# Optimization experiments

Measured on AMD Instinct MI355X. Metric: run time of the kernel, lower is better.

The kernel has to match this reference:

```python
import jax, jax.numpy as jnp
import numpy as np

B, C, Q, T, D = 16, 6, 256, 256, 256
NUM_IDS = 300
IMG_H = IMG_W = 512


def setup_inputs() -> dict:
    key = jax.random.key(0)
    ks = jax.random.split(key, 8)
    det_tokens = jax.random.normal(ks[0], (B, C, Q, D), jnp.float32)
    det_scores = jax.random.uniform(ks[1], (B, C, Q), jnp.float32)
    det_boxes = jax.random.uniform(ks[2], (B, C, Q, 4), jnp.float32)
    assoc = jax.nn.softmax(jax.random.normal(ks[3], (B, C, Q, T), jnp.float32), axis=-1)
    cam_mask = jax.random.uniform(ks[4], (B, C)) < 0.9
    target_mask = jax.random.uniform(ks[5], (B, C, Q)) < 0.5
    ids = jax.random.randint(ks[6], (B, C, Q), 0, NUM_IDS)
    boxes = jax.random.uniform(ks[7], (B, C, Q, 4), jnp.float32) * IMG_W
    return {"det_tokens": det_tokens, "det_scores": det_scores, "det_boxes": det_boxes,
            "assoc": assoc, "boxes": boxes, "cam_mask": cam_mask,
            "target_mask": target_mask, "ids": ids, "img_h": IMG_H, "img_w": IMG_W}


def _masked_mean(x, m):
    w = m.astype(x.dtype)
    return (x * w).sum() / jnp.maximum(w.sum(), 1.0)


def _pack(ids, target_mask, cam_mask, q_count):
    # Vectorized version of _query_ids_from_targets: stable-compact valid targets
    # to the front of the query axis (preserves original order, as boolean indexing does).
    order = jnp.argsort(jnp.where(target_mask, 0, 1), axis=-1, stable=True)  # valid first
    sids = jnp.take_along_axis(ids, order, axis=-1)[..., :q_count]
    count = target_mask.sum(axis=-1)  # [B,C]
    qvalid = (jnp.arange(q_count)[None, None, :] < count[..., None]) & cam_mask[..., None]
    qids = jnp.where(qvalid, sids, -1)
    return qids, qvalid, order


def reference(det_tokens, det_scores, det_boxes, assoc, boxes, cam_mask, target_mask, ids, img_h, img_w):
    Bq, Cc, Qn, Tn = assoc.shape
    qids, qvalid, order = _pack(ids, target_mask, cam_mask, Qn)

    # det_norm
    det_norm = jnp.mean(det_tokens ** 2)

    # detector supervision (masked BCE on scores + masked L1 on boxes)
    norm = jnp.array([img_w, img_h, img_w, img_h], det_boxes.dtype)
    box_gt = boxes / norm  # [B,C,maxT,4]
    sboxes = jnp.take_along_axis(box_gt, order[..., None], axis=2)[:, :, :Qn]
    obj_target = qvalid.astype(det_scores.dtype)
    box_target = jnp.where(qvalid[..., None], jnp.clip(sboxes, 0.0, 1.0), 0.0)
    p = jnp.clip(det_scores, 1e-6, 1.0 - 1e-6)
    bce = -(obj_target * jnp.log(p) + (1.0 - obj_target) * jnp.log1p(-p))
    cam3 = jnp.broadcast_to(cam_mask[:, :, None], bce.shape)
    score_loss = _masked_mean(bce, cam3)
    box_loss = _masked_mean(jnp.abs(det_boxes - box_target),
                            jnp.broadcast_to(qvalid[..., None], det_boxes.shape))
    det_supervision = score_loss + box_loss

    # assoc entropy (masked by camera validity)
    logp_full = jnp.log(jnp.maximum(assoc, 1e-8))
    entropy = -(logp_full * assoc).sum(-1)  # [B,C,Q]
    assoc_entropy_loss = _masked_mean(entropy, jnp.broadcast_to(cam_mask[:, :, None], entropy.shape))

    # assoc supervised NLL over track slots
    slots = jnp.remainder(jnp.maximum(qids, 0), Tn)  # [B,C,Q]
    nll = -jnp.take_along_axis(logp_full, slots[..., None], axis=-1)[..., 0]
    assoc_pair_loss = _masked_mean(nll, qvalid)

    # cross-view consistency: broadcasted id-equality replaces quadruple python loop
    eq = qids[:, :, None, :, None] == qids[:, None, :, None, :]       # [B,c1,c2,q1,q2]
    pv = qvalid[:, :, None, :, None] & qvalid[:, None, :, None, :]
    tri = jnp.triu(jnp.ones((Cc, Cc), bool), 1)[None, :, :, None, None]  # c1 < c2
    M = (eq & pv & tri).astype(assoc.dtype)
    cnt = M.sum(-1)  # [B,c1,c2,q1]
    peer = jnp.einsum('bcdqp,bdpt->bcdqt', M, assoc) / jnp.maximum(cnt, 1.0)[..., None]
    ref = assoc[:, :, None, :, :]
    term = jnp.mean((ref - peer) ** 2, axis=-1)  # per-pair MSE over track slots
    assoc_consistency = _masked_mean(term, cnt > 0)

    total = det_norm + det_supervision + assoc_entropy_loss + assoc_pair_loss + assoc_consistency
    return total, det_norm, det_supervision, assoc_entropy_loss, assoc_pair_loss, assoc_consistency
```

## Files before the change

### kernel.cpp

```cpp
#include <hip/hip_runtime.h>
#include <math.h>

#define BB 16
#define CC 6
#define QQ 256
#define TT 256
#define DD 256
#define NPAIR 15
#define NBC (BB * CC)
#define BIG_BLOCKS (NBC * 16)
#define CONS_BLOCKS (BB * NPAIR * 4)


__device__ __forceinline__ float block_sum256(float v, float* s_red) {
    #pragma unroll
    for (int off = 32; off > 0; off >>= 1) v += __shfl_xor(v, off, 64);
    __syncthreads();
    if ((threadIdx.x & 63) == 0) s_red[threadIdx.x >> 6] = v;
    __syncthreads();
    return s_red[0] + s_red[1] + s_red[2] + s_red[3];
}

__device__ __forceinline__ int read_bool(const void* p, int idx, int fmt) {
    if (fmt == 2) return ((const float*)p)[idx] != 0.0f;
    if (fmt == 1) return ((const unsigned char*)p)[idx] != 0;
    return ((const int*)p)[idx] != 0;
}

__global__ __launch_bounds__(256)
void k_pack(const float* __restrict__ det_scores,
            const float* __restrict__ det_boxes,
            const float* __restrict__ assoc,
            const float* __restrict__ boxes,
            const void* __restrict__ cam_raw,
            const void* __restrict__ tm_raw,
            const int* __restrict__ ids,
            const int* __restrict__ img_h_p,
            const int* __restrict__ img_w_p,
            unsigned char* __restrict__ cam_c,
            int* __restrict__ qids,
            float* __restrict__ packPart) {
    const int bc = blockIdx.x;
    const int t = threadIdx.x;
    const int lane = t & 63, wv = t >> 6;
    __shared__ int s_cf, s_cm, s_wsum[4];
    __shared__ int s_sids[QQ];
    __shared__ float s_red[4];

    if (t == 0) { s_cf = 0; s_cm = 0; }
    __syncthreads();
    {
        uint4 w = ((const uint4*)tm_raw)[t];
        unsigned int u4[4] = {w.x, w.y, w.z, w.w};
        int cf = 0, cm = 0;
        #pragma unroll
        for (int k = 0; k < 4; k++) {
            cf += ((u4[k] >> 24) == 0x3Fu);
            cm += ((u4[k] & 0xFFFFFF00u) != 0u);
        }
        if (cf) atomicAdd(&s_cf, cf);
        if (cm) atomicAdd(&s_cm, cm);
    }
    __syncthreads();
    const int fmt = (s_cf > 16) ? 2 : ((s_cm > 0) ? 1 : 0);

    const int cam = read_bool(cam_raw, bc, fmt);
    const int tm  = read_bool(tm_raw, bc * QQ + t, fmt);
    if (t == 0) cam_c[bc] = (unsigned char)cam;

    int v = tm;
    #pragma unroll
    for (int off = 1; off < 64; off <<= 1) {
        int u = __shfl_up(v, off, 64);
        if (lane >= off) v += u;
    }
    if (lane == 63) s_wsum[wv] = v;
    __syncthreads();
    const int count = s_wsum[0] + s_wsum[1] + s_wsum[2] + s_wsum[3];
    int woff = 0;
    #pragma unroll
    for (int k = 0; k < 3; k++) woff += (k < wv) ? s_wsum[k] : 0;
    const int excl = woff + v - tm;
    const int rank = tm ? excl : (count + (t - excl));

    s_sids[rank] = ids[bc * QQ + t];
    __syncthreads();

    const int j = t;
    const int qv = (j < count) && cam;
    const int qid = qv ? s_sids[j] : -1;
    qids[bc * QQ + j] = qid;

    float score_sum = 0.0f, box_sum = 0.0f, pair_sum = 0.0f;

    if (cam) {
        float p = det_scores[(size_t)bc * QQ + j];
        p = fminf(fmaxf(p, 1e-6f), 1.0f - 1e-6f);
        score_sum = (j < count) ? -__logf(p) : -__logf(1.0f - p);
    }
    if (qv) {
        int slot = qid & (TT - 1);
        float a = assoc[((size_t)bc * QQ + j) * TT + slot];
        pair_sum = -__logf(fmaxf(a, 1e-8f));
    }
    if (tm && cam) {
        const int jj = rank;
        const float iw = (float)img_w_p[0], ih = (float)img_h_p[0];
        const float* bx = boxes + ((size_t)bc * QQ + t) * 4;
        const float* db = det_boxes + ((size_t)bc * QQ + jj) * 4;
        float b0 = fminf(fmaxf(bx[0] / iw, 0.0f), 1.0f);
        float b1 = fminf(fmaxf(bx[1] / ih, 0.0f), 1.0f);
        float b2 = fminf(fmaxf(bx[2] / iw, 0.0f), 1.0f);
        float b3 = fminf(fmaxf(bx[3] / ih, 0.0f), 1.0f);
        box_sum = fabsf(db[0] - b0) + fabsf(db[1] - b1) +
                  fabsf(db[2] - b2) + fabsf(db[3] - b3);
    }

    float vs = block_sum256(score_sum, s_red);
    float vb = block_sum256(box_sum, s_red);
    float vp = block_sum256(pair_sum, s_red);
    if (t == 0) {
        float* row = packPart + bc * 8;
        row[0] = vs; row[1] = vb; row[2] = vp;
        row[3] = cam ? (float)count : 0.0f;
        row[4] = (float)cam;
    }
}

__global__ __launch_bounds__(256)
void k_big(const float4* __restrict__ tok, const float4* __restrict__ asc,
           const unsigned char* __restrict__ cam_c, float* __restrict__ bigPart) {
    const int blk = blockIdx.x;
    const int bc = blk >> 4;
    const int t = threadIdx.x;
    const long base = (long)bc * 16384 + (long)(blk & 15) * 1024 + t;

    float4 t0 = tok[base], t1 = tok[base + 256],
           t2 = tok[base + 512], t3 = tok[base + 768];
    float ss = t0.x * t0.x + t0.y * t0.y + t0.z * t0.z + t0.w * t0.w
             + t1.x * t1.x + t1.y * t1.y + t1.z * t1.z + t1.w * t1.w
             + t2.x * t2.x + t2.y * t2.y + t2.z * t2.z + t2.w * t2.w
             + t3.x * t3.x + t3.y * t3.y + t3.z * t3.z + t3.w * t3.w;

    float ent = 0.0f;
    if (cam_c[bc]) {
        float4 a0 = asc[base], a1 = asc[base + 256],
               a2 = asc[base + 512], a3 = asc[base + 768];
        ent -= a0.x * __logf(fmaxf(a0.x, 1e-8f)) + a0.y * __logf(fmaxf(a0.y, 1e-8f))
             + a0.z * __logf(fmaxf(a0.z, 1e-8f)) + a0.w * __logf(fmaxf(a0.w, 1e-8f));
        ent -= a1.x * __logf(fmaxf(a1.x, 1e-8f)) + a1.y * __logf(fmaxf(a1.y, 1e-8f))
             + a1.z * __logf(fmaxf(a1.z, 1e-8f)) + a1.w * __logf(fmaxf(a1.w, 1e-8f));
        ent -= a2.x * __logf(fmaxf(a2.x, 1e-8f)) + a2.y * __logf(fmaxf(a2.y, 1e-8f))
             + a2.z * __logf(fmaxf(a2.z, 1e-8f)) + a2.w * __logf(fmaxf(a2.w, 1e-8f));
        ent -= a3.x * __logf(fmaxf(a3.x, 1e-8f)) + a3.y * __logf(fmaxf(a3.y, 1e-8f))
             + a3.z * __logf(fmaxf(a3.z, 1e-8f)) + a3.w * __logf(fmaxf(a3.w, 1e-8f));
    }

    __shared__ float s_red[4];
    float vss = block_sum256(ss, s_red);
    float vent = block_sum256(ent, s_red);
    if (t == 0) { bigPart[blk * 2] = vss; bigPart[blk * 2 + 1] = vent; }
}

__global__ __launch_bounds__(256)
void k_cons(const float* __restrict__ assoc, const int* __restrict__ qids,
            float* __restrict__ consPart) {
    const int blk = blockIdx.x;
    const int qg = blk & 3;
    const int bp = blk >> 2;
    const int b = bp / NPAIR;
    int pi = bp % NPAIR;
    int c = 0, d = 1;
    {
        int k = pi;
        for (c = 0; c < CC - 1; c++) {
            int span = CC - 1 - c;
            if (k < span) { d = c + 1 + k; break; }
            k -= span;
        }
    }
    const int t = threadIdx.x, lane = t & 63, wv = t >> 6;
    __shared__ int s_qc[64];
    __shared__ int s_qd[QQ];
    __shared__ float s_wred[4];
    __shared__ int s_wnval[4];
    if (t < 64) s_qc[t] = qids[(b * CC + c) * QQ + qg * 64 + t];
    s_qd[t] = qids[(b * CC + d) * QQ + t];
    __syncthreads();

    const int qd0 = s_qd[lane];
    const int qd1 = s_qd[64 + lane];
    const int qd2 = s_qd[128 + lane];
    const int qd3 = s_qd[192 + lane];
    const float4* assoc_c = (const float4*)(assoc + (size_t)(b * CC + c) * QQ * TT);
    const float4* assoc_d = (const float4*)(assoc + (size_t)(b * CC + d) * QQ * TT);

    float tot = 0.0f;
    int nval = 0;
    for (int qi = 0; qi < 16; qi++) {
        const int qloc = wv * 16 + qi;
        const int id = s_qc[qloc];
        if (id < 0) continue;
        unsigned long long m0 = __ballot(qd0 == id);
        unsigned long long m1 = __ballot(qd1 == id);
        unsigned long long m2 = __ballot(qd2 == id);
        unsigned long long m3 = __ballot(qd3 == id);
        int cnt = __popcll(m0) + __popcll(m1) + __popcll(m2) + __popcll(m3);
        if (cnt == 0) continue;
        const int q = qg * 64 + qloc;
        float4 r = assoc_c[(size_t)q * (TT / 4) + lane];
        float ax = 0.0f, ay = 0.0f, az = 0.0f, aw = 0.0f;
        unsigned long long mm[4] = {m0, m1, m2, m3};
        #pragma unroll
        for (int kk = 0; kk < 4; kk++) {
            unsigned long long m = mm[kk];
            while (m) {
                int p = kk * 64 + __builtin_ctzll(m);
                m &= m - 1;
                float4 vv = assoc_d[(size_t)p * (TT / 4) + lane];
                ax += vv.x; ay += vv.y; az += vv.z; aw += vv.w;
            }
        }
        float inv = 1.0f / (float)cnt;
        float dx = r.x - ax * inv, dy = r.y - ay * inv;
        float dz = r.z - az * inv, dw = r.w - aw * inv;
        tot += dx * dx + dy * dy + dz * dz + dw * dw;
        nval++;
    }
    #pragma unroll
    for (int off = 32; off > 0; off >>= 1) tot += __shfl_xor(tot, off, 64);
    if (lane == 0) { s_wred[wv] = tot; s_wnval[wv] = nval; }
    __syncthreads();
    if (t == 0) {
        float csum = s_wred[0] + s_wred[1] + s_wred[2] + s_wred[3];
        int n4 = s_wnval[0] + s_wnval[1] + s_wnval[2] + s_wnval[3];
        consPart[blk * 2] = csum * (1.0f / TT);
        consPart[blk * 2 + 1] = (float)n4;
    }
}

__global__ __launch_bounds__(256)
void k_fin(const float* __restrict__ packPart, const float* __restrict__ bigPart,
           const float* __restrict__ consPart, float* __restrict__ out) {
    const int t = threadIdx.x;
    __shared__ float s_red[4];
    float sc = 0, bx = 0, pr = 0, qv = 0, cm = 0;
    if (t < NBC) {
        const float* row = packPart + t * 8;
        sc = row[0]; bx = row[1]; pr = row[2]; qv = row[3]; cm = row[4];
    }
    float ss = 0, ent = 0;
    for (int i = t; i < BIG_BLOCKS; i += 256) {
        ss += bigPart[2 * i]; ent += bigPart[2 * i + 1];
    }
    float cons = 0, nval = 0;
    for (int i = t; i < CONS_BLOCKS; i += 256) {
        cons += consPart[2 * i]; nval += consPart[2 * i + 1];
    }
    sc = block_sum256(sc, s_red);
    bx = block_sum256(bx, s_red);
    pr = block_sum256(pr, s_red);
    qv = block_sum256(qv, s_red);
    cm = block_sum256(cm, s_red);
    ss = block_sum256(ss, s_red);
    ent = block_sum256(ent, s_red);
    cons = block_sum256(cons, s_red);
    nval = block_sum256(nval, s_red);
    if (t == 0) {
        float det_norm = ss / (float)((long)BB * CC * QQ * DD);
        float denom_cam = fmaxf(cm * (float)QQ, 1.0f);
        float score_loss = sc / denom_cam;
        float box_loss = bx / fmaxf(4.0f * qv, 1.0f);
        float det_sup = score_loss + box_loss;
        float ent_loss = ent / denom_cam;
        float pair_loss = pr / fmaxf(qv, 1.0f);
        float cons_loss = cons / fmaxf(nval, 1.0f);
        out[0] = det_norm + det_sup + ent_loss + pair_loss + cons_loss;
        out[1] = det_norm;
        out[2] = det_sup;
        out[3] = ent_loss;
        out[4] = pair_loss;
        out[5] = cons_loss;
    }
}

extern "C" void kernel_launch(void* const* d_in, const int* in_sizes, int n_in,
                              void* d_out, int out_size, void* d_ws, size_t ws_size,
                              hipStream_t stream) {
    const float* det_tokens = (const float*)d_in[0];
    const float* det_scores = (const float*)d_in[1];
    const float* det_boxes  = (const float*)d_in[2];
    const float* assoc      = (const float*)d_in[3];
    const float* boxes      = (const float*)d_in[4];
    const void*  cam_raw    = d_in[5];
    const void*  tm_raw     = d_in[6];
    const int*   ids        = (const int*)d_in[7];
    const int*   img_h      = (const int*)d_in[8];
    const int*   img_w      = (const int*)d_in[9];

    char* ws = (char*)d_ws;
    int* qids            = (int*)(ws + 0);
    unsigned char* cam_c = (unsigned char*)(ws + 98304);
    float* packPart      = (float*)(ws + 98432);
    float* bigPart       = (float*)(ws + 101504);
    float* consPart      = (float*)(ws + 113792);

    k_pack<<<NBC, 256, 0, stream>>>(det_scores, det_boxes, assoc, boxes,
                                    cam_raw, tm_raw, ids, img_h, img_w,
                                    cam_c, qids, packPart);
    k_big<<<BIG_BLOCKS, 256, 0, stream>>>((const float4*)det_tokens,
                                          (const float4*)assoc, cam_c, bigPart);
    k_cons<<<CONS_BLOCKS, 256, 0, stream>>>(assoc, qids, consPart);
    k_fin<<<1, 256, 0, stream>>>(packPart, bigPart, consPart, (float*)d_out);
}
```

Before: 120.2 us.

## Merge big, consistency and final reduction kernels via last-block ticket

Fuses the det-norm/entropy streaming kernel and the cross-view consistency kernel into one launch by splitting on block index. The final reduction kernel is folded in using an atomic ticket counter, so only the last finishing block performs it. The ticket is reset inside the pack kernel. This removes two kernel launches and lets the two independent workloads overlap on the device, at the cost of a threadfence and an atomic in every block.

```diff
diff --git a/kernel.cpp b/kernel.cpp
--- a/kernel.cpp
+++ b/kernel.cpp
@@ -10,6 +10,7 @@
 #define NBC (BB * CC)
 #define BIG_BLOCKS (NBC * 16)
 #define CONS_BLOCKS (BB * NPAIR * 4)
+#define MAIN_BLOCKS (BIG_BLOCKS + CONS_BLOCKS)
 
 
 __device__ __forceinline__ float block_sum256(float v, float* s_red) {
@@ -39,13 +40,16 @@
             const int* __restrict__ img_w_p,
             unsigned char* __restrict__ cam_c,
             int* __restrict__ qids,
-            float* __restrict__ packPart) {
+            float* __restrict__ packPart,
+            int* __restrict__ ticket) {
     const int bc = blockIdx.x;
     const int t = threadIdx.x;
     const int lane = t & 63, wv = t >> 6;
     __shared__ int s_cf, s_cm, s_wsum[4];
     __shared__ int s_sids[QQ];
     __shared__ float s_red[4];
+
+    if (bc == 0 && t == 0) ticket[0] = 0;
 
     if (t == 0) { s_cf = 0; s_cm = 0; }
     __syncthreads();
@@ -128,122 +132,128 @@
 }
 
 __global__ __launch_bounds__(256)
-void k_big(const float4* __restrict__ tok, const float4* __restrict__ asc,
-           const unsigned char* __restrict__ cam_c, float* __restrict__ bigPart) {
+void k_main(const float4* __restrict__ tok, const float* __restrict__ assoc,
+            const unsigned char* __restrict__ cam_c,
+            const int* __restrict__ qids,
+            float* __restrict__ packPart, float* __restrict__ bigPart,
+            float* __restrict__ consPart, int* __restrict__ ticket,
+            float* __restrict__ out) {
     const int blk = blockIdx.x;
-    const int bc = blk >> 4;
-    const int t = threadIdx.x;
-    const long base = (long)bc * 16384 + (long)(blk & 15) * 1024 + t;
-
-    float4 t0 = tok[base], t1 = tok[base + 256],
-           t2 = tok[base + 512], t3 = tok[base + 768];
-    float ss = t0.x * t0.x + t0.y * t0.y + t0.z * t0.z + t0.w * t0.w
-             + t1.x * t1.x + t1.y * t1.y + t1.z * t1.z + t1.w * t1.w
-             + t2.x * t2.x + t2.y * t2.y + t2.z * t2.z + t2.w * t2.w
-             + t3.x * t3.x + t3.y * t3.y + t3.z * t3.z + t3.w * t3.w;
-
-    float ent = 0.0f;
-    if (cam_c[bc]) {
-        float4 a0 = asc[base], a1 = asc[base + 256],
-               a2 = asc[base + 512], a3 = asc[base + 768];
-        ent -= a0.x * __logf(fmaxf(a0.x, 1e-8f)) + a0.y * __logf(fmaxf(a0.y, 1e-8f))
-             + a0.z * __logf(fmaxf(a0.z, 1e-8f)) + a0.w * __logf(fmaxf(a0.w, 1e-8f));
-        ent -= a1.x * __logf(fmaxf(a1.x, 1e-8f)) + a1.y * __logf(fmaxf(a1.y, 1e-8f))
-             + a1.z * __logf(fmaxf(a1.z, 1e-8f)) + a1.w * __logf(fmaxf(a1.w, 1e-8f));
-        ent -= a2.x * __logf(fmaxf(a2.x, 1e-8f)) + a2.y * __logf(fmaxf(a2.y, 1e-8f))
-             + a2.z * __logf(fmaxf(a2.z, 1e-8f)) + a2.w * __logf(fmaxf(a2.w, 1e-8f));
-        ent -= a3.x * __logf(fmaxf(a3.x, 1e-8f)) + a3.y * __logf(fmaxf(a3.y, 1e-8f))
-             + a3.z * __logf(fmaxf(a3.z, 1e-8f)) + a3.w * __logf(fmaxf(a3.w, 1e-8f));
-    }
-
+    const int t = threadIdx.x, lane = t & 63, wv = t >> 6;
     __shared__ float s_red[4];
-    float vss = block_sum256(ss, s_red);
-    float vent = block_sum256(ent, s_red);
-    if (t == 0) { bigPart[blk * 2] = vss; bigPart[blk * 2 + 1] = vent; }
-}
-
-__global__ __launch_bounds__(256)
-void k_cons(const float* __restrict__ assoc, const int* __restrict__ qids,
-            float* __restrict__ consPart) {
-    const int blk = blockIdx.x;
-    const int qg = blk & 3;
-    const int bp = blk >> 2;
-    const int b = bp / NPAIR;
-    int pi = bp % NPAIR;
-    int c = 0, d = 1;
-    {
-        int k = pi;
-        for (c = 0; c < CC - 1; c++) {
-            int span = CC - 1 - c;
-            if (k < span) { d = c + 1 + k; break; }
-            k -= span;
-        }
-    }
-    const int t = threadIdx.x, lane = t & 63, wv = t >> 6;
-    __shared__ int s_qc[64];
-    __shared__ int s_qd[QQ];
-    __shared__ float s_wred[4];
-    __shared__ int s_wnval[4];
-    if (t < 64) s_qc[t] = qids[(b * CC + c) * QQ + qg * 64 + t];
-    s_qd[t] = qids[(b * CC + d) * QQ + t];
-    __syncthreads();
-
-    const int qd0 = s_qd[lane];
-    const int qd1 = s_qd[64 + lane];
-    const int qd2 = s_qd[128 + lane];
-    const int qd3 = s_qd[192 + lane];
-    const float4* assoc_c = (const float4*)(assoc + (size_t)(b * CC + c) * QQ * TT);
-    const float4* assoc_d = (const float4*)(assoc + (size_t)(b * CC + d) * QQ * TT);
-
-    float tot = 0.0f;
-    int nval = 0;
-    for (int qi = 0; qi < 16; qi++) {
-        const int qloc = wv * 16 + qi;
-        const int id = s_qc[qloc];
-        if (id < 0) continue;
-        unsigned long long m0 = __ballot(qd0 == id);
-        unsigned long long m1 = __ballot(qd1 == id);
-        unsigned long long m2 = __ballot(qd2 == id);
-        unsigned long long m3 = __ballot(qd3 == id);
-        int cnt = __popcll(m0) + __popcll(m1) + __popcll(m2) + __popcll(m3);
-        if (cnt == 0) continue;
-        const int q = qg * 64 + qloc;
-        float4 r = assoc_c[(size_t)q * (TT / 4) + lane];
-        float ax = 0.0f, ay = 0.0f, az = 0.0f, aw = 0.0f;
-        unsigned long long mm[4] = {m0, m1, m2, m3};
+
+    if (blk < BIG_BLOCKS) {
+        const int bc = blk >> 4;
+        const long base = (long)bc * 16384 + (long)(blk & 15) * 1024 + t;
+        const float4* asc = (const float4*)assoc;
+
+        float4 t0 = tok[base], t1 = tok[base + 256],
+               t2 = tok[base + 512], t3 = tok[base + 768];
+        float ss = t0.x * t0.x + t0.y * t0.y + t0.z * t0.z + t0.w * t0.w
+                 + t1.x * t1.x + t1.y * t1.y + t1.z * t1.z + t1.w * t1.w
+                 + t2.x * t2.x + t2.y * t2.y + t2.z * t2.z + t2.w * t2.w
+                 + t3.x * t3.x + t3.y * t3.y + t3.z * t3.z + t3.w * t3.w;
+
+        float ent = 0.0f;
+        if (cam_c[bc]) {
+            float4 a0 = asc[base], a1 = asc[base + 256],
+                   a2 = asc[base + 512], a3 = asc[base + 768];
+            ent -= a0.x * __logf(fmaxf(a0.x, 1e-8f)) + a0.y * __logf(fmaxf(a0.y, 1e-8f))
+                 + a0.z * __logf(fmaxf(a0.z, 1e-8f)) + a0.w * __logf(fmaxf(a0.w, 1e-8f));
+            ent -= a1.x * __logf(fmaxf(a1.x, 1e-8f)) + a1.y * __logf(fmaxf(a1.y, 1e-8f))
+                 + a1.z * __logf(fmaxf(a1.z, 1e-8f)) + a1.w * __logf(fmaxf(a1.w, 1e-8f));
+            ent -= a2.x * __logf(fmaxf(a2.x, 1e-8f)) + a2.y * __logf(fmaxf(a2.y, 1e-8f))
+                 + a2.z * __logf(fmaxf(a2.z, 1e-8f)) + a2.w * __logf(fmaxf(a2.w, 1e-8f));
+            ent -= a3.x * __logf(fmaxf(a3.x, 1e-8f)) + a3.y * __logf(fmaxf(a3.y, 1e-8f))
+                 + a3.z * __logf(fmaxf(a3.z, 1e-8f)) + a3.w * __logf(fmaxf(a3.w, 1e-8f));
+        }
+        float vss = block_sum256(ss, s_red);
+        float vent = block_sum256(ent, s_red);
+        if (t == 0) { bigPart[blk * 2] = vss; bigPart[blk * 2 + 1] = vent; }
+    } else {
+        const int cb = blk - BIG_BLOCKS;
+        const int qg = cb & 3;
+        const int bp = cb >> 2;
+        const int b = bp / NPAIR;
+        int pi = bp % NPAIR;
+        int c = 0, d = 1;
+        {
+            int k = pi;
+            for (c = 0; c < CC - 1; c++) {
+                int span = CC - 1 - c;
+                if (k < span) { d = c + 1 + k; break; }
+                k -= span;
+            }
+        }
+        __shared__ int s_qc[64];
+        __shared__ int s_qd[QQ];
+        __shared__ int s_wnval[4];
+        if (t < 64) s_qc[t] = qids[(b * CC + c) * QQ + qg * 64 + t];
+        s_qd[t] = qids[(b * CC + d) * QQ + t];
+        __syncthreads();
+
+        const int qd0 = s_qd[lane];
+        const int qd1 = s_qd[64 + lane];
+        const int qd2 = s_qd[128 + lane];
+        const int qd3 = s_qd[192 + lane];
+        const float4* assoc_c = (const float4*)(assoc + (size_t)(b * CC + c) * QQ * TT);
+        const float4* assoc_d = (const float4*)(assoc + (size_t)(b * CC + d) * QQ * TT);
+
+        float tot = 0.0f;
+        int nval = 0;
+        for (int qi = 0; qi < 16; qi++) {
+            const int qloc = wv * 16 + qi;
+            const int id = s_qc[qloc];
+            if (id < 0) continue;
+            unsigned long long m0 = __ballot(qd0 == id);
+            unsigned long long m1 = __ballot(qd1 == id);
+            unsigned long long m2 = __ballot(qd2 == id);
+            unsigned long long m3 = __ballot(qd3 == id);
+            int cnt = __popcll(m0) + __popcll(m1) + __popcll(m2) + __popcll(m3);
+            if (cnt == 0) continue;
+            const int q = qg * 64 + qloc;
+            float4 r = assoc_c[(size_t)q * (TT / 4) + lane];
+            float ax = 0.0f, ay = 0.0f, az = 0.0f, aw = 0.0f;
+            unsigned long long mm[4] = {m0, m1, m2, m3};
+            #pragma unroll
+            for (int kk = 0; kk < 4; kk++) {
+                unsigned long long m = mm[kk];
+                while (m) {
+                    int p = kk * 64 + __builtin_ctzll(m);
+                    m &= m - 1;
+                    float4 vv = assoc_d[(size_t)p * (TT / 4) + lane];
+                    ax += vv.x; ay += vv.y; az += vv.z; aw += vv.w;
+                }
+            }
+            float inv = 1.0f / (float)cnt;
+            float dx = r.x - ax * inv, dy = r.y - ay * inv;
+            float dz = r.z - az * inv, dw = r.w - aw * inv;
+            tot += dx * dx + dy * dy + dz * dz + dw * dw;
+            nval++;
+        }
         #pragma unroll
-        for (int kk = 0; kk < 4; kk++) {
-            unsigned long long m = mm[kk];
-            while (m) {
-                int p = kk * 64 + __builtin_ctzll(m);
-                m &= m - 1;
-                float4 vv = assoc_d[(size_t)p * (TT / 4) + lane];
-                ax += vv.x; ay += vv.y; az += vv.z; aw += vv.w;
-            }
-        }
-        float inv = 1.0f / (float)cnt;
-        float dx = r.x - ax * inv, dy = r.y - ay * inv;
-        float dz = r.z - az * inv, dw = r.w - aw * inv;
-        tot += dx * dx + dy * dy + dz * dz + dw * dw;
-        nval++;
-    }
-    #pragma unroll
-    for (int off = 32; off > 0; off >>= 1) tot += __shfl_xor(tot, off, 64);
-    if (lane == 0) { s_wred[wv] = tot; s_wnval[wv] = nval; }
+        for (int off = 32; off > 0; off >>= 1) tot += __shfl_xor(tot, off, 64);
+        if (lane == 0) { s_red[wv] = tot; s_wnval[wv] = nval; }
+        __syncthreads();
+        if (t == 0) {
+            float csum = s_red[0] + s_red[1] + s_red[2] + s_red[3];
+            int n4 = s_wnval[0] + s_wnval[1] + s_wnval[2] + s_wnval[3];
+            consPart[cb * 2] = csum * (1.0f / TT);
+            consPart[cb * 2 + 1] = (float)n4;
+        }
+    }
+
+    __shared__ int s_last;
+    __threadfence();
     __syncthreads();
     if (t == 0) {
-        float csum = s_wred[0] + s_wred[1] + s_wred[2] + s_wred[3];
-        int n4 = s_wnval[0] + s_wnval[1] + s_wnval[2] + s_wnval[3];
-        consPart[blk * 2] = csum * (1.0f / TT);
-        consPart[blk * 2 + 1] = (float)n4;
-    }
-}
-
-__global__ __launch_bounds__(256)
-void k_fin(const float* __restrict__ packPart, const float* __restrict__ bigPart,
-           const float* __restrict__ consPart, float* __restrict__ out) {
-    const int t = threadIdx.x;
-    __shared__ float s_red[4];
+        int old = atomicAdd(ticket, 1);
+        s_last = (old == MAIN_BLOCKS - 1);
+    }
+    __syncthreads();
+    if (!s_last) return;
+    __threadfence();
+
     float sc = 0, bx = 0, pr = 0, qv = 0, cm = 0;
     if (t < NBC) {
         const float* row = packPart + t * 8;
@@ -302,14 +312,14 @@
     int* qids            = (int*)(ws + 0);
     unsigned char* cam_c = (unsigned char*)(ws + 98304);
     float* packPart      = (float*)(ws + 98432);
-    float* bigPart       = (float*)(ws + 101504);
-    float* consPart      = (float*)(ws + 113792);
+    int* ticket          = (int*)(ws + 101504);
+    float* bigPart       = (float*)(ws + 101632);
+    float* consPart      = (float*)(ws + 113920);
 
     k_pack<<<NBC, 256, 0, stream>>>(det_scores, det_boxes, assoc, boxes,
                                     cam_raw, tm_raw, ids, img_h, img_w,
-                                    cam_c, qids, packPart);
-    k_big<<<BIG_BLOCKS, 256, 0, stream>>>((const float4*)det_tokens,
-                                          (const float4*)assoc, cam_c, bigPart);
-    k_cons<<<CONS_BLOCKS, 256, 0, stream>>>(assoc, qids, consPart);
-    k_fin<<<1, 256, 0, stream>>>(packPart, bigPart, consPart, (float*)d_out);
-}
+                                    cam_c, qids, packPart, ticket);
+    k_main<<<MAIN_BLOCKS, 256, 0, stream>>>((const float4*)det_tokens, assoc,
+                                            cam_c, qids, packPart, bigPart,
+                                            consPart, ticket, (float*)d_out);
+}
```

Measured after the change: 333.9 us. +177.8%, slower.
